# Performance work log

Measured on AMD Instinct MI355X. Metric: run time of the kernel, lower is better.

The kernel has to match this reference:

```python
import jax, jax.numpy as jnp
import numpy as np

C = 128        # attention channels (inner_channel)
OUT_C = 256    # bottleneck output channels (in_channel)
NEG = -10000000.0


def conv_bn_relu(x, W, scale, shift):
    """1x1 conv (no bias) + eval-mode BatchNorm folded to scale/shift + ReLU.
    x: [B, Cin, H, W], W: [Cout, Cin]."""
    y = jnp.einsum('oc,bchw->bohw', W, x)
    y = y * scale[None, :, None, None] + shift[None, :, None, None]
    return jax.nn.relu(y)


def setup_inputs() -> dict:
    key = jax.random.key(0)
    ks = jax.random.split(key, 20)
    B, H, W_, K = 4, 128, 128, 1024
    inp = {
        'query_feats': jax.random.normal(ks[0], (B, C, H, W_), jnp.float32),
        'key_feats':   jax.random.normal(ks[1], (B, C, K, 1), jnp.float32),
        'value_feats': jax.random.normal(ks[2], (B, C, K, 1), jnp.float32),
        'key_mask':    jax.random.randint(ks[3], (B, 1, K, 1), 0, 2).astype(bool),
    }
    s = 1.0 / np.sqrt(C)

    def mk(i, cin, cout):
        return (jax.random.normal(ks[i], (cout, cin), jnp.float32) * s,
                jnp.ones((cout,), jnp.float32),
                jnp.zeros((cout,), jnp.float32))

    inp['Wq1'], inp['sq1'], inp['bq1'] = mk(4, C, C)
    inp['Wq2'], inp['sq2'], inp['bq2'] = mk(5, C, C)
    inp['Wk1'], inp['sk1'], inp['bk1'] = mk(6, C, C)
    inp['Wk2'], inp['sk2'], inp['bk2'] = mk(7, C, C)
    inp['Wv'],  inp['sv'],  inp['bv']  = mk(8, C, C)
    inp['Wo'],  inp['so'],  inp['bo']  = mk(9, C, C)
    inp['Wb'],  inp['sb'],  inp['bb']  = mk(10, 2 * C, OUT_C)
    return inp


def reference(query_feats, key_feats, value_feats, key_mask,
              Wq1, sq1, bq1, Wq2, sq2, bq2,
              Wk1, sk1, bk1, Wk2, sk2, bk2,
              Wv, sv, bv, Wo, so, bo, Wb, sb, bb):
    B, _, H, W_ = query_feats.shape
    # projections (2 conv-bn-relu for q/k, 1 for v)
    q = conv_bn_relu(conv_bn_relu(query_feats, Wq1, sq1, bq1), Wq2, sq2, bq2)
    k = conv_bn_relu(conv_bn_relu(key_feats, Wk1, sk1, bk1), Wk2, sk2, bk2)
    v = conv_bn_relu(value_feats, Wv, sv, bv)

    q = q.reshape(B, C, -1).transpose(0, 2, 1)   # [B, HW, C]
    k = k.reshape(B, C, -1)                      # [B, C, K]
    v = v.reshape(B, C, -1).transpose(0, 2, 1)   # [B, K, C]

    sim = jnp.einsum('bqc,bck->bqk', q, k) * (C ** -0.5)   # [B, HW, K]
    m = key_mask.reshape(B, 1, -1).astype(sim.dtype)        # [B, 1, K]
    sim = sim * m + NEG * (1.0 - m)
    attn = jax.nn.softmax(sim, axis=-1)

    ctx = jnp.einsum('bqk,bkc->bqc', attn, v)               # [B, HW, C]
    ctx = ctx.transpose(0, 2, 1).reshape(B, C, H, W_)
    ctx = conv_bn_relu(ctx, Wo, so, bo)                     # out_project

    out = conv_bn_relu(jnp.concatenate([ctx, query_feats], axis=1), Wb, sb, bb)
    return out
```

## Files before the change

### kernel.cpp

```cpp
#include <hip/hip_runtime.h>
#include <hip/hip_bf16.h>

#define B_    4
#define C_    128
#define HW_   16384
#define K_    1024
#define SC2_  0.12751734f
#define NEGL_ (-1.4427e7f)
#define DTHR_ 8.0f

using bf16 = __hip_bfloat16;
typedef __bf16 b8v __attribute__((ext_vector_type(8)));
typedef __bf16 b4v __attribute__((ext_vector_type(4)));
typedef __bf16 b2v __attribute__((ext_vector_type(2)));
typedef float  f4v __attribute__((ext_vector_type(4)));

__device__ __forceinline__ b8v ldb8(const void* p) { return *(const b8v*)p; }

#define XSTRIDE 272
#define KSTRIDE 272
#define VSTRIDE 144

__device__ __forceinline__ b8v ldw8(const float* wp, float sc) {
    const float4 a = *(const float4*)wp;
    const float4 c = *(const float4*)(wp + 4);
    b8v r;
    r[0] = (__bf16)(a.x * sc); r[1] = (__bf16)(a.y * sc);
    r[2] = (__bf16)(a.z * sc); r[3] = (__bf16)(a.w * sc);
    r[4] = (__bf16)(c.x * sc); r[5] = (__bf16)(c.y * sc);
    r[6] = (__bf16)(c.z * sc); r[7] = (__bf16)(c.w * sc);
    return r;
}

__global__ __launch_bounds__(256, 2) void prep_kernel(
    const float* __restrict__ query, const float* __restrict__ key, const float* __restrict__ val,
    const float* __restrict__ Wq1, const float* __restrict__ sq1,
    const float* __restrict__ Wq2, const float* __restrict__ sq2,
    const float* __restrict__ Wo,  const float* __restrict__ so,
    const float* __restrict__ Wb,  const float* __restrict__ sb,
    const float* __restrict__ Wk1, const float* __restrict__ sk1, const float* __restrict__ bk1,
    const float* __restrict__ Wk2, const float* __restrict__ sk2, const float* __restrict__ bk2,
    const float* __restrict__ Wv,  const float* __restrict__ sv_, const float* __restrict__ bv,
    bf16* __restrict__ qt, bf16* __restrict__ kbuf, bf16* __restrict__ vbuf,
    __bf16* __restrict__ Wq1p, __bf16* __restrict__ Wq2p,
    __bf16* __restrict__ Wop,  __bf16* __restrict__ Wbp)
{
    __shared__ __align__(16) char SM[69632];
    const int blk = blockIdx.x, t = threadIdx.x;

    if (blk < 32) {
        const int b = blk >> 3, n0 = (blk & 7) * 128;
        const int w = t >> 6, lane = t & 63;
        const int pl = lane & 15, quad = lane >> 4;
        const int ob = 32 * w;
        const int plT = t & 63, cg = t >> 6;
        char*    Xs  = SM;
        __bf16*  Ys  = (__bf16*)(SM + 34816);
        float*   Tmp = (float*)(SM + 34816);

        auto transpose_in = [&](const float* src) {
#pragma unroll
            for (int h = 0; h < 2; ++h) {
                const int p0 = n0 + h * 64;
#pragma unroll 4
                for (int i2 = 0; i2 < 32; ++i2) {
                    const int c = cg * 32 + i2;
                    Tmp[plT * 129 + c] = src[(size_t)(b * 128 + c) * K_ + p0 + plT];
                }
                __syncthreads();
#pragma unroll 4
                for (int it = 0; it < 16; ++it) {
                    const int p = it * 4 + cg;
                    b2v pk2;
                    pk2[0] = (__bf16)Tmp[p * 129 + 2 * plT];
                    pk2[1] = (__bf16)Tmp[p * 129 + 2 * plT + 1];
                    *(b2v*)(Xs + (h * 64 + p) * XSTRIDE + 4 * plT) = pk2;
                }
                __syncthreads();
            }
        };

        transpose_in(key);
        b8v W1f[2][4], W2f[2][4];
#pragma unroll
        for (int mt = 0; mt < 2; ++mt)
#pragma unroll
            for (int s = 0; s < 4; ++s) {
                const int row = ob + mt * 16 + pl;
                W1f[mt][s] = ldw8(Wk1 + row * 128 + s * 32 + quad * 8, sk1[row]);
                W2f[mt][s] = ldw8(Wk2 + row * 128 + s * 32 + quad * 8, sk2[row]);
            }
        {
            f4v acc[2][8];
#pragma unroll
            for (int mt = 0; mt < 2; ++mt)
#pragma unroll
                for (int nt = 0; nt < 8; ++nt) acc[mt][nt] = (f4v){0.f, 0.f, 0.f, 0.f};
#pragma unroll
            for (int s = 0; s < 4; ++s) {
                b8v Bf[8];
#pragma unroll
                for (int nt = 0; nt < 8; ++nt)
                    Bf[nt] = ldb8(Xs + (nt * 16 + pl) * XSTRIDE + s * 64 + quad * 16);
#pragma unroll
                for (int mt = 0; mt < 2; ++mt)
#pragma unroll
                    for (int nt = 0; nt < 8; ++nt)
                        acc[mt][nt] = __builtin_amdgcn_mfma_f32_16x16x32_bf16(W1f[mt][s], Bf[nt], acc[mt][nt], 0, 0, 0);
            }
#pragma unroll
            for (int mt = 0; mt < 2; ++mt) {
                const float4 s4 = *(const float4*)(bk1 + ob + mt * 16 + quad * 4);
                const float shf[4] = {s4.x, s4.y, s4.z, s4.w};
#pragma unroll
                for (int nt = 0; nt < 8; ++nt) {
                    b4v y;
#pragma unroll
                    for (int r = 0; r < 4; ++r) y[r] = (__bf16)fmaxf(acc[mt][nt][r] + shf[r], 0.f);
                    *(b4v*)&Ys[(nt * 16 + pl) * 136 + ob + mt * 16 + quad * 4] = y;
                }
            }
        }
        __syncthreads();
        {
            f4v acc2[2][8];
#pragma unroll
            for (int mt = 0; mt < 2; ++mt)
#pragma unroll
                for (int nt = 0; nt < 8; ++nt) acc2[mt][nt] = (f4v){0.f, 0.f, 0.f, 0.f};
#pragma unroll
            for (int s = 0; s < 4; ++s) {
                b8v Bf[8];
#pragma unroll
                for (int nt = 0; nt < 8; ++nt)
                    Bf[nt] = *(const b8v*)&Ys[(nt * 16 + pl) * 136 + s * 32 + quad * 8];
#pragma unroll
                for (int mt = 0; mt < 2; ++mt)
#pragma unroll
                    for (int nt = 0; nt < 8; ++nt)
                        acc2[mt][nt] = __builtin_amdgcn_mfma_f32_16x16x32_bf16(W2f[mt][s], Bf[nt], acc2[mt][nt], 0, 0, 0);
            }
            bf16* kdst = kbuf + ((size_t)b * K_ + n0) * 128;
#pragma unroll
            for (int mt = 0; mt < 2; ++mt) {
                const float4 s4 = *(const float4*)(bk2 + ob + mt * 16 + quad * 4);
                const float shf[4] = {s4.x, s4.y, s4.z, s4.w};
#pragma unroll
                for (int nt = 0; nt < 8; ++nt) {
                    b4v y;
#pragma unroll
                    for (int r = 0; r < 4; ++r) y[r] = (__bf16)fmaxf(acc2[mt][nt][r] + shf[r], 0.f);
                    *(b4v*)(kdst + (size_t)(nt * 16 + pl) * 128 + ob + mt * 16 + quad * 4) = y;
                }
            }
        }
        __syncthreads();

        transpose_in(val);
        b8v Wvf[2][4];
#pragma unroll
        for (int mt = 0; mt < 2; ++mt)
#pragma unroll
            for (int s = 0; s < 4; ++s) {
                const int row = ob + mt * 16 + pl;
                Wvf[mt][s] = ldw8(Wv + row * 128 + s * 32 + quad * 8, sv_[row]);
            }
        {
            f4v acc[2][8];
#pragma unroll
            for (int mt = 0; mt < 2; ++mt)
#pragma unroll
                for (int nt = 0; nt < 8; ++nt) acc[mt][nt] = (f4v){0.f, 0.f, 0.f, 0.f};
#pragma unroll
            for (int s = 0; s < 4; ++s) {
                b8v Bf[8];
#pragma unroll
                for (int nt = 0; nt < 8; ++nt)
                    Bf[nt] = ldb8(Xs + (nt * 16 + pl) * XSTRIDE + s * 64 + quad * 16);
#pragma unroll
                for (int mt = 0; mt < 2; ++mt)
#pragma unroll
                    for (int nt = 0; nt < 8; ++nt)
                        acc[mt][nt] = __builtin_amdgcn_mfma_f32_16x16x32_bf16(Wvf[mt][s], Bf[nt], acc[mt][nt], 0, 0, 0);
            }
            bf16* vdst = vbuf + (size_t)b * 128 * K_;
#pragma unroll
            for (int mt = 0; mt < 2; ++mt) {
                const float4 s4 = *(const float4*)(bv + ob + mt * 16 + quad * 4);
                const float shf[4] = {s4.x, s4.y, s4.z, s4.w};
#pragma unroll
                for (int nt = 0; nt < 8; ++nt)
#pragma unroll
                    for (int r = 0; r < 4; ++r)
                        vdst[(size_t)(ob + mt * 16 + quad * 4 + r) * K_ + n0 + nt * 16 + pl]
                            = __float2bfloat16(fmaxf(acc[mt][nt][r] + shf[r], 0.f));
            }
        }
    } else if (blk < 1056) {
        float* Xs2 = (float*)SM;
        const int i = blk - 32;
        const int b = i >> 8, p0 = (i & 255) * 64;
        const int pl = t & 63, cg = t >> 6;
#pragma unroll 4
        for (int i2 = 0; i2 < 32; ++i2) {
            const int c = cg * 32 + i2;
            Xs2[pl * 129 + c] = query[(size_t)(b * 128 + c) * HW_ + p0 + pl];
        }
        __syncthreads();
#pragma unroll 4
        for (int it = 0; it < 16; ++it) {
            const int p = it * 4 + cg;
            b2v pk2;
            pk2[0] = (__bf16)Xs2[p * 129 + 2 * pl];
            pk2[1] = (__bf16)Xs2[p * 129 + 2 * pl + 1];
            *(b2v*)(qt + ((size_t)b * HW_ + p0 + p) * 128 + 2 * pl) = pk2;
        }
    } else {
        const int idx = (blk - 1056) * 256 + t;
        if (idx < 16384)      { Wq1p[idx] = (__bf16)(Wq1[idx] * sq1[idx >> 7]); }
        else if (idx < 32768) { const int i2 = idx - 16384; Wq2p[i2] = (__bf16)(Wq2[i2] * sq2[i2 >> 7]); }
        else if (idx < 49152) { const int i2 = idx - 32768; Wop[i2]  = (__bf16)(Wo[i2]  * so[i2 >> 7]); }
        else                  { const int i2 = idx - 49152; Wbp[i2]  = (__bf16)(Wb[i2]  * sb[i2 >> 8]); }
    }
}

__global__ __launch_bounds__(256, 2) void mega_kernel(
    const bf16* __restrict__ qt, const bf16* __restrict__ kbuf, const bf16* __restrict__ vbuf,
    const int* __restrict__ mask,
    const __bf16* __restrict__ Wq1p, const float* __restrict__ bq1,
    const __bf16* __restrict__ Wq2p, const float* __restrict__ bq2,
    const __bf16* __restrict__ Wop,  const float* __restrict__ bo,
    const __bf16* __restrict__ Wbp,  const float* __restrict__ bb,
    float* __restrict__ out)
{
    __shared__ __align__(16) char S[75776];

    const int t = threadIdx.x, w = t >> 6, lane = t & 63;
    const int pl = lane & 15, quad = lane >> 4;
    const int n0 = blockIdx.x * 128;
    const int b  = blockIdx.y;
    const int ob = 32 * w;

    char*   RA  = S;
    __bf16* RAh = (__bf16*)S;
    __bf16* RBh = (__bf16*)(S + 34816);
    char* xl = RA + (t >> 4) * XSTRIDE + (t & 15) * 16;

    {
        const char* qg = (const char*)(qt + ((size_t)b * HW_ + n0) * 128) + t * 16;
#pragma unroll
        for (int i = 0; i < 8; ++i)
            *(float4*)(xl + i * 16 * XSTRIDE) = *(const float4*)(qg + i * 4096);
    }
    {
        b8v W1f[2][4], W2f[2][4];
#pragma unroll
        for (int mt = 0; mt < 2; ++mt)
#pragma unroll
            for (int s = 0; s < 4; ++s) {
                W1f[mt][s] = ldb8(Wq1p + (ob + mt * 16 + pl) * 128 + s * 32 + quad * 8);
                W2f[mt][s] = ldb8(Wq2p + (ob + mt * 16 + pl) * 128 + s * 32 + quad * 8);
            }
        __syncthreads();

        f4v a1[2][8];
#pragma unroll
        for (int mt = 0; mt < 2; ++mt)
#pragma unroll
            for (int nt = 0; nt < 8; ++nt) a1[mt][nt] = (f4v){0.f, 0.f, 0.f, 0.f};
#pragma unroll
        for (int s = 0; s < 4; ++s) {
            b8v Bf[8];
#pragma unroll
            for (int nt = 0; nt < 8; ++nt)
                Bf[nt] = ldb8(RA + (nt * 16 + pl) * XSTRIDE + s * 64 + quad * 16);
#pragma unroll
            for (int mt = 0; mt < 2; ++mt)
#pragma unroll
                for (int nt = 0; nt < 8; ++nt)
                    a1[mt][nt] = __builtin_amdgcn_mfma_f32_16x16x32_bf16(W1f[mt][s], Bf[nt], a1[mt][nt], 0, 0, 0);
        }
#pragma unroll
        for (int mt = 0; mt < 2; ++mt) {
            const float4 s4 = *(const float4*)(bq1 + ob + mt * 16 + quad * 4);
            const float shf[4] = {s4.x, s4.y, s4.z, s4.w};
#pragma unroll
            for (int nt = 0; nt < 8; ++nt) {
                b4v y;
#pragma unroll
                for (int r = 0; r < 4; ++r) y[r] = (__bf16)fmaxf(a1[mt][nt][r] + shf[r], 0.f);
                *(b4v*)&RBh[(nt * 16 + pl) * 136 + ob + mt * 16 + quad * 4] = y;
            }
        }
        __syncthreads();

        f4v a2[2][8];
#pragma unroll
        for (int mt = 0; mt < 2; ++mt)
#pragma unroll
            for (int nt = 0; nt < 8; ++nt) a2[mt][nt] = (f4v){0.f, 0.f, 0.f, 0.f};
#pragma unroll
        for (int s = 0; s < 4; ++s) {
            b8v Bf[8];
#pragma unroll
            for (int nt = 0; nt < 8; ++nt)
                Bf[nt] = *(const b8v*)&RBh[(nt * 16 + pl) * 136 + s * 32 + quad * 8];
#pragma unroll
            for (int mt = 0; mt < 2; ++mt)
#pragma unroll
                for (int nt = 0; nt < 8; ++nt)
                    a2[mt][nt] = __builtin_amdgcn_mfma_f32_16x16x32_bf16(W2f[mt][s], Bf[nt], a2[mt][nt], 0, 0, 0);
        }
#pragma unroll
        for (int mt = 0; mt < 2; ++mt) {
            const float4 s4 = *(const float4*)(bq2 + ob + mt * 16 + quad * 4);
            const float shf[4] = {s4.x, s4.y, s4.z, s4.w};
#pragma unroll
            for (int nt = 0; nt < 8; ++nt) {
                b4v y;
#pragma unroll
                for (int r = 0; r < 4; ++r) y[r] = (__bf16)fmaxf(a2[mt][nt][r] + shf[r], 0.f);
                *(b4v*)&RAh[(nt * 16 + pl) * 136 + ob + mt * 16 + quad * 4] = y;
            }
        }
        __syncthreads();
    }

    b8v qf0[4], qf1[4];
#pragma unroll
    for (int s = 0; s < 4; ++s) {
        qf0[s] = ldb8(RA + (w * 32 + pl) * XSTRIDE + s * 64 + quad * 16);
        qf1[s] = ldb8(RA + (w * 32 + 16 + pl) * XSTRIDE + s * 64 + quad * 16);
    }
    __syncthreads();

    float* bias = (float*)S;
    char* kt0 = S + 4096;
    char* kt1 = S + 21504;
    char* vt0 = S + 38912;
    char* vt1 = S + 57344;

    const bf16* kpt = kbuf + (size_t)b * K_ * 128;
    const bf16* vpt = vbuf + (size_t)b * 128 * K_;
    const char* kg = (const char*)kpt + t * 16;
    const char* vg = (const char*)(vpt + (size_t)(t >> 3) * K_) + (t & 7) * 16;
    const int klo = (t >> 4) * KSTRIDE + (t & 15) * 16;
    const int vj  = t & 7;
    const int vlo = (t >> 3) * VSTRIDE + (vj >> 2) * 64 + (vj & 1) * 32 + ((vj >> 1) & 1) * 8;

    float4 kr[4], vr[4];

#define ISSUE_LOADS(chunk)                                            \
    { const char* kgn = kg + (chunk) * 16384;                         \
      const char* vgn = vg + (chunk) * 128;                           \
      kr[0] = *(const float4*)(kgn);                                  \
      kr[1] = *(const float4*)(kgn + 4096);                           \
      kr[2] = *(const float4*)(kgn + 8192);                           \
      kr[3] = *(const float4*)(kgn + 12288);                          \
      vr[0] = *(const float4*)(vgn);                                  \
      vr[1] = *(const float4*)(vgn + 65536);                          \
      vr[2] = *(const float4*)(vgn + 131072);                         \
      vr[3] = *(const float4*)(vgn + 196608); }

#define STAGE_WRITES(ktd, vtd)                                        \
    { char* klp = (ktd) + klo;                                        \
      *(float4*)(klp)                = kr[0];                         \
      *(float4*)(klp + 16 * KSTRIDE) = kr[1];                         \
      *(float4*)(klp + 32 * KSTRIDE) = kr[2];                         \
      *(float4*)(klp + 48 * KSTRIDE) = kr[3];                         \
      char* vlp = (vtd) + vlo;                                        \
      *(float2*)(vlp)                     = make_float2(vr[0].x, vr[0].y); \
      *(float2*)(vlp + 16)                = make_float2(vr[0].z, vr[0].w); \
      *(float2*)(vlp + 32 * VSTRIDE)      = make_float2(vr[1].x, vr[1].y); \
      *(float2*)(vlp + 32 * VSTRIDE + 16) = make_float2(vr[1].z, vr[1].w); \
      *(float2*)(vlp + 64 * VSTRIDE)      = make_float2(vr[2].x, vr[2].y); \
      *(float2*)(vlp + 64 * VSTRIDE + 16) = make_float2(vr[2].z, vr[2].w); \
      *(float2*)(vlp + 96 * VSTRIDE)      = make_float2(vr[3].x, vr[3].y); \
      *(float2*)(vlp + 96 * VSTRIDE + 16) = make_float2(vr[3].z, vr[3].w); }

#define RAW_BARRIER()                                                 \
    __builtin_amdgcn_sched_barrier(0);                                \
    asm volatile("s_waitcnt lgkmcnt(0)" ::: "memory");                \
    __builtin_amdgcn_s_barrier();                                     \
    __builtin_amdgcn_sched_barrier(0);

    ISSUE_LOADS(0)
    for (int i2 = t; i2 < K_; i2 += 256)
        bias[i2] = (mask[b * K_ + i2] != 0) ? 0.f : NEGL_;
    STAGE_WRITES(kt0, vt0)
    ISSUE_LOADS(1)

    f4v ac0[8], ac1[8];
#pragma unroll
    for (int i = 0; i < 8; ++i) { ac0[i] = (f4v){0.f,0.f,0.f,0.f}; ac1[i] = (f4v){0.f,0.f,0.f,0.f}; }
    float mrun0 = -3.0e38f, mrun1 = -3.0e38f, lrun0 = 0.f, lrun1 = 0.f;

    RAW_BARRIER()

#pragma unroll 2
    for (int ch = 0; ch < 16; ++ch) {
        const char* ktc = (ch & 1) ? kt1 : kt0;
        const char* vtc = (ch & 1) ? vt1 : vt0;
        const int k0 = ch * 64;

        f4v sv0[4], sv1[4];
        __builtin_amdgcn_s_setprio(1);
#pragma unroll
        for (int kt = 0; kt < 4; ++kt) {
            f4v a0 = (f4v){0.f,0.f,0.f,0.f}, a1 = (f4v){0.f,0.f,0.f,0.f};
            const char* krow = ktc + (kt * 16 + pl) * KSTRIDE + quad * 16;
#pragma unroll
            for (int s = 0; s < 4; ++s) {
                const b8v kf = ldb8(krow + s * 64);
                a0 = __builtin_amdgcn_mfma_f32_16x16x32_bf16(kf, qf0[s], a0, 0, 0, 0);
                a1 = __builtin_amdgcn_mfma_f32_16x16x32_bf16(kf, qf1[s], a1, 0, 0, 0);
            }
            const float4 b4 = *(const float4*)&bias[k0 + kt * 16 + quad * 4];
            const float bb4[4] = {b4.x, b4.y, b4.z, b4.w};
#pragma unroll
            for (int r = 0; r < 4; ++r) { sv0[kt][r] = a0[r] * SC2_ + bb4[r];
                                          sv1[kt][r] = a1[r] * SC2_ + bb4[r]; }
        }
        __builtin_amdgcn_s_setprio(0);

        if (ch < 15) {
            if (ch & 1) { STAGE_WRITES(kt0, vt0) } else { STAGE_WRITES(kt1, vt1) }
            if (ch < 14) ISSUE_LOADS(ch + 2)
        }

        float ml0 = sv0[0][0], ml1 = sv1[0][0];
#pragma unroll
        for (int kt = 0; kt < 4; ++kt)
#pragma unroll
            for (int r = 0; r < 4; ++r) { ml0 = fmaxf(ml0, sv0[kt][r]); ml1 = fmaxf(ml1, sv1[kt][r]); }
        ml0 = fmaxf(ml0, __shfl_xor(ml0, 16, 64)); ml0 = fmaxf(ml0, __shfl_xor(ml0, 32, 64));
        ml1 = fmaxf(ml1, __shfl_xor(ml1, 16, 64)); ml1 = fmaxf(ml1, __shfl_xor(ml1, 32, 64));

        if (__any((ml0 > mrun0 + DTHR_) || (ml1 > mrun1 + DTHR_))) {
            const float mn0 = fmaxf(mrun0, ml0), mn1 = fmaxf(mrun1, ml1);
            const float al0 = exp2f(mrun0 - mn0), al1 = exp2f(mrun1 - mn1);
            lrun0 *= al0; lrun1 *= al1;
            mrun0 = mn0;  mrun1 = mn1;
            float ar0[4], ar1[4];
#pragma unroll
            for (int r = 0; r < 4; ++r) { ar0[r] = __shfl(al0, quad * 4 + r, 64);
                                          ar1[r] = __shfl(al1, quad * 4 + r, 64); }
#pragma unroll
            for (int ct = 0; ct < 8; ++ct)
#pragma unroll
                for (int r = 0; r < 4; ++r) { ac0[ct][r] *= ar0[r]; ac1[ct][r] *= ar1[r]; }
        }

        b4v pk0[4], pk1[4];
        float rs0 = 0.f, rs1 = 0.f;
#pragma unroll
        for (int kt = 0; kt < 4; ++kt)
#pragma unroll
            for (int r = 0; r < 4; ++r) {
                const float p0 = exp2f(sv0[kt][r] - mrun0); rs0 += p0; pk0[kt][r] = (__bf16)p0;
                const float p1 = exp2f(sv1[kt][r] - mrun1); rs1 += p1; pk1[kt][r] = (__bf16)p1;
            }
        rs0 += __shfl_xor(rs0, 16, 64); rs0 += __shfl_xor(rs0, 32, 64);
        rs1 += __shfl_xor(rs1, 16, 64); rs1 += __shfl_xor(rs1, 32, 64);
        lrun0 += rs0; lrun1 += rs1;

        const b8v A00 = __builtin_shufflevector(pk0[0], pk0[1], 0, 1, 2, 3, 4, 5, 6, 7);
        const b8v A01 = __builtin_shufflevector(pk0[2], pk0[3], 0, 1, 2, 3, 4, 5, 6, 7);
        const b8v A10 = __builtin_shufflevector(pk1[0], pk1[1], 0, 1, 2, 3, 4, 5, 6, 7);
        const b8v A11 = __builtin_shufflevector(pk1[2], pk1[3], 0, 1, 2, 3, 4, 5, 6, 7);
        __builtin_amdgcn_s_setprio(1);
#pragma unroll
        for (int ct = 0; ct < 8; ++ct) {
            const char* vrow = vtc + (ct * 16 + pl) * VSTRIDE + quad * 16;
            const b8v B0 = ldb8(vrow);
            const b8v B1 = ldb8(vrow + 64);
            ac0[ct] = __builtin_amdgcn_mfma_f32_16x16x32_bf16(A00, B0, ac0[ct], 0, 0, 0);
            ac0[ct] = __builtin_amdgcn_mfma_f32_16x16x32_bf16(A01, B1, ac0[ct], 0, 0, 0);
            ac1[ct] = __builtin_amdgcn_mfma_f32_16x16x32_bf16(A10, B0, ac1[ct], 0, 0, 0);
            ac1[ct] = __builtin_amdgcn_mfma_f32_16x16x32_bf16(A11, B1, ac1[ct], 0, 0, 0);
        }
        __builtin_amdgcn_s_setprio(0);

        RAW_BARRIER()
    }
#undef ISSUE_LOADS
#undef STAGE_WRITES
#undef RAW_BARRIER

    {
        float inv0[4], inv1[4];
#pragma unroll
        for (int r = 0; r < 4; ++r) { inv0[r] = 1.f / __shfl(lrun0, quad * 4 + r, 64);
                                      inv1[r] = 1.f / __shfl(lrun1, quad * 4 + r, 64); }
#pragma unroll
        for (int ct = 0; ct < 8; ++ct)
#pragma unroll
            for (int r = 0; r < 4; ++r) {
                RAh[(w * 32 + quad * 4 + r) * 136 + ct * 16 + pl]      = (__bf16)(ac0[ct][r] * inv0[r]);
                RAh[(w * 32 + 16 + quad * 4 + r) * 136 + ct * 16 + pl] = (__bf16)(ac1[ct][r] * inv1[r]);
            }
    }
    __syncthreads();

    b8v Wof[2][4];
#pragma unroll
    for (int mt = 0; mt < 2; ++mt)
#pragma unroll
        for (int s = 0; s < 4; ++s)
            Wof[mt][s] = ldb8(Wop + (ob + mt * 16 + pl) * 128 + s * 32 + quad * 8);

    const char* qg2 = (const char*)(qt + ((size_t)b * HW_ + n0) * 128) + t * 16;
    float4 q_s0 = *(const float4*)(qg2);
    float4 q_s1 = *(const float4*)(qg2 + 4096);
    float4 q_s2 = *(const float4*)(qg2 + 8192);
    float4 q_s3 = *(const float4*)(qg2 + 12288);
    float4 q_s4 = *(const float4*)(qg2 + 16384);
    float4 q_s5 = *(const float4*)(qg2 + 20480);
    float4 q_s6 = *(const float4*)(qg2 + 24576);
    float4 q_s7 = *(const float4*)(qg2 + 28672);

    {
        f4v f1[2][8];
#pragma unroll
        for (int mt = 0; mt < 2; ++mt)
#pragma unroll
            for (int nt = 0; nt < 8; ++nt) f1[mt][nt] = (f4v){0.f, 0.f, 0.f, 0.f};
#pragma unroll
        for (int s = 0; s < 4; ++s) {
            b8v Bf[8];
#pragma unroll
            for (int nt = 0; nt < 8; ++nt)
                Bf[nt] = ldb8(RA + (nt * 16 + pl) * XSTRIDE + s * 64 + quad * 16);
#pragma unroll
            for (int mt = 0; mt < 2; ++mt)
#pragma unroll
                for (int nt = 0; nt < 8; ++nt)
                    f1[mt][nt] = __builtin_amdgcn_mfma_f32_16x16x32_bf16(Wof[mt][s], Bf[nt], f1[mt][nt], 0, 0, 0);
        }
#pragma unroll
        for (int mt = 0; mt < 2; ++mt) {
            const float4 s4 = *(const float4*)(bo + ob + mt * 16 + quad * 4);
            const float shf[4] = {s4.x, s4.y, s4.z, s4.w};
#pragma unroll
            for (int nt = 0; nt < 8; ++nt) {
                b4v y;
#pragma unroll
                for (int r = 0; r < 4; ++r) y[r] = (__bf16)fmaxf(f1[mt][nt][r] + shf[r], 0.f);
                *(b4v*)&RBh[(nt * 16 + pl) * 136 + ob + mt * 16 + quad * 4] = y;
            }
        }
    }
    __syncthreads();

    *(float4*)(xl)                 = q_s0;
    *(float4*)(xl + 16 * XSTRIDE)  = q_s1;
    *(float4*)(xl + 32 * XSTRIDE)  = q_s2;
    *(float4*)(xl + 48 * XSTRIDE)  = q_s3;
    *(float4*)(xl + 64 * XSTRIDE)  = q_s4;
    *(float4*)(xl + 80 * XSTRIDE)  = q_s5;
    *(float4*)(xl + 96 * XSTRIDE)  = q_s6;
    *(float4*)(xl + 112 * XSTRIDE) = q_s7;
    __syncthreads();

    {
        f4v f2[4][8];
#pragma unroll
        for (int mt = 0; mt < 4; ++mt)
#pragma unroll
            for (int nt = 0; nt < 8; ++nt) f2[mt][nt] = (f4v){0.f, 0.f, 0.f, 0.f};
#pragma unroll
        for (int ks = 0; ks < 8; ++ks) {
            b8v Af[4];
#pragma unroll
            for (int mt = 0; mt < 4; ++mt)
                Af[mt] = ldb8(Wbp + (size_t)(64 * w + mt * 16 + pl) * 256 + ks * 32 + quad * 8);
            b8v Bf[8];
            if (ks < 4) {
#pragma unroll
                for (int nt = 0; nt < 8; ++nt)
                    Bf[nt] = *(const b8v*)&RBh[(nt * 16 + pl) * 136 + ks * 32 + quad * 8];
            } else {
#pragma unroll
                for (int nt = 0; nt < 8; ++nt)
                    Bf[nt] = ldb8(RA + (nt * 16 + pl) * XSTRIDE + (ks - 4) * 64 + quad * 16);
            }
#pragma unroll
            for (int mt = 0; mt < 4; ++mt)
#pragma unroll
                for (int nt = 0; nt < 8; ++nt)
                    f2[mt][nt] = __builtin_amdgcn_mfma_f32_16x16x32_bf16(Af[mt], Bf[nt], f2[mt][nt], 0, 0, 0);
        }
#pragma unroll
        for (int mt = 0; mt < 4; ++mt) {
            const float4 s4 = *(const float4*)(bb + 64 * w + mt * 16 + quad * 4);
            const float shf[4] = {s4.x, s4.y, s4.z, s4.w};
#pragma unroll
            for (int nt = 0; nt < 8; ++nt)
#pragma unroll
                for (int r = 0; r < 4; ++r)
                    out[(size_t)(b * 256 + 64 * w + mt * 16 + quad * 4 + r) * HW_ + n0 + nt * 16 + pl]
                        = fmaxf(f2[mt][nt][r] + shf[r], 0.f);
        }
    }
}

extern "C" void kernel_launch(void* const* d_in, const int* in_sizes, int n_in,
                              void* d_out, int out_size, void* d_ws, size_t ws_size,
                              hipStream_t stream)
{
    const float* query = (const float*)d_in[0];
    const float* key   = (const float*)d_in[1];
    const float* val   = (const float*)d_in[2];
    const int*   mask  = (const int*)  d_in[3];
    const float* Wq1 = (const float*)d_in[4];  const float* sq1 = (const float*)d_in[5];  const float* bq1 = (const float*)d_in[6];
    const float* Wq2 = (const float*)d_in[7];  const float* sq2 = (const float*)d_in[8];  const float* bq2 = (const float*)d_in[9];
    const float* Wk1 = (const float*)d_in[10]; const float* sk1 = (const float*)d_in[11]; const float* bk1 = (const float*)d_in[12];
    const float* Wk2 = (const float*)d_in[13]; const float* sk2 = (const float*)d_in[14]; const float* bk2 = (const float*)d_in[15];
    const float* Wv  = (const float*)d_in[16]; const float* sv  = (const float*)d_in[17]; const float* bv  = (const float*)d_in[18];
    const float* Wo  = (const float*)d_in[19]; const float* so  = (const float*)d_in[20]; const float* bo  = (const float*)d_in[21];
    const float* Wb  = (const float*)d_in[22]; const float* sb  = (const float*)d_in[23]; const float* bb  = (const float*)d_in[24];

    char* ws = (char*)d_ws;
    bf16*   qt   = (bf16*)(ws);
    bf16*   kbuf = (bf16*)(ws + (16u << 20));
    bf16*   vbuf = (bf16*)(ws + (17u << 20));
    char*   wbase = ws + (18u << 20);
    __bf16* Wq1p = (__bf16*)(wbase);
    __bf16* Wq2p = (__bf16*)(wbase + (32u << 10));
    __bf16* Wop  = (__bf16*)(wbase + (64u << 10));
    __bf16* Wbp  = (__bf16*)(wbase + (96u << 10));
    float* outp = (float*)d_out;

    prep_kernel<<<1504, 256, 0, stream>>>(
        query, key, val,
        Wq1, sq1, Wq2, sq2, Wo, so, Wb, sb,
        Wk1, sk1, bk1, Wk2, sk2, bk2, Wv, sv, bv,
        qt, kbuf, vbuf, Wq1p, Wq2p, Wop, Wbp);
    mega_kernel<<<dim3(HW_ / 128, B_), 256, 0, stream>>>(
        qt, kbuf, vbuf, mask,
        Wq1p, bq1, Wq2p, bq2, Wop, bo, Wbp, bb, outp);
}
```

Before: 231.7 us.

## Replace double-buffered K/V LDS staging with single buffer and register prefetch

Drops the two-slot LDS ping-pong for K and V tiles and uses one LDS tile per operand. Each chunk's data, held in registers, is written to LDS and followed by a barrier before the next chunk's global loads are issued. The V tile switches from a permuted 8-byte-store layout to plain 16-byte stores with a smaller stride, and reads it back as two 4-element loads per operand. This cuts LDS use and store instruction count, but adds a barrier per chunk and shortens the overlap of global loads with compute.

```diff
diff --git a/kernel.cpp b/kernel.cpp
--- a/kernel.cpp
+++ b/kernel.cpp
@@ -16,10 +16,11 @@
 typedef float  f4v __attribute__((ext_vector_type(4)));
 
 __device__ __forceinline__ b8v ldb8(const void* p) { return *(const b8v*)p; }
+__device__ __forceinline__ b4v ldb4(const void* p) { return *(const b4v*)p; }
 
 #define XSTRIDE 272
 #define KSTRIDE 272
-#define VSTRIDE 144
+#define VSTRIDE 136
 
 __device__ __forceinline__ b8v ldw8(const float* wp, float sc) {
     const float4 a = *(const float4*)wp;
@@ -233,7 +234,7 @@
     const __bf16* __restrict__ Wbp,  const float* __restrict__ bb,
     float* __restrict__ out)
 {
-    __shared__ __align__(16) char S[75776];
+    __shared__ __align__(16) char S[69632];
 
     const int t = threadIdx.x, w = t >> 6, lane = t & 63;
     const int pl = lane & 15, quad = lane >> 4;
@@ -335,48 +336,32 @@
     __syncthreads();
 
     float* bias = (float*)S;
-    char* kt0 = S + 4096;
-    char* kt1 = S + 21504;
-    char* vt0 = S + 38912;
-    char* vt1 = S + 57344;
+    char* ktile = S + 4096;
+    char* vtile = S + 34816;
+
+    for (int i2 = t; i2 < K_; i2 += 256)
+        bias[i2] = (mask[b * K_ + i2] != 0) ? 0.f : NEGL_;
 
     const bf16* kpt = kbuf + (size_t)b * K_ * 128;
     const bf16* vpt = vbuf + (size_t)b * 128 * K_;
     const char* kg = (const char*)kpt + t * 16;
     const char* vg = (const char*)(vpt + (size_t)(t >> 3) * K_) + (t & 7) * 16;
-    const int klo = (t >> 4) * KSTRIDE + (t & 15) * 16;
-    const int vj  = t & 7;
-    const int vlo = (t >> 3) * VSTRIDE + (vj >> 2) * 64 + (vj & 1) * 32 + ((vj >> 1) & 1) * 8;
-
-    float4 kr[4], vr[4];
-
-#define ISSUE_LOADS(chunk)                                            \
-    { const char* kgn = kg + (chunk) * 16384;                         \
-      const char* vgn = vg + (chunk) * 128;                           \
-      kr[0] = *(const float4*)(kgn);                                  \
-      kr[1] = *(const float4*)(kgn + 4096);                           \
-      kr[2] = *(const float4*)(kgn + 8192);                           \
-      kr[3] = *(const float4*)(kgn + 12288);                          \
-      vr[0] = *(const float4*)(vgn);                                  \
-      vr[1] = *(const float4*)(vgn + 65536);                          \
-      vr[2] = *(const float4*)(vgn + 131072);                         \
-      vr[3] = *(const float4*)(vgn + 196608); }
-
-#define STAGE_WRITES(ktd, vtd)                                        \
-    { char* klp = (ktd) + klo;                                        \
-      *(float4*)(klp)                = kr[0];                         \
-      *(float4*)(klp + 16 * KSTRIDE) = kr[1];                         \
-      *(float4*)(klp + 32 * KSTRIDE) = kr[2];                         \
-      *(float4*)(klp + 48 * KSTRIDE) = kr[3];                         \
-      char* vlp = (vtd) + vlo;                                        \
-      *(float2*)(vlp)                     = make_float2(vr[0].x, vr[0].y); \
-      *(float2*)(vlp + 16)                = make_float2(vr[0].z, vr[0].w); \
-      *(float2*)(vlp + 32 * VSTRIDE)      = make_float2(vr[1].x, vr[1].y); \
-      *(float2*)(vlp + 32 * VSTRIDE + 16) = make_float2(vr[1].z, vr[1].w); \
-      *(float2*)(vlp + 64 * VSTRIDE)      = make_float2(vr[2].x, vr[2].y); \
-      *(float2*)(vlp + 64 * VSTRIDE + 16) = make_float2(vr[2].z, vr[2].w); \
-      *(float2*)(vlp + 96 * VSTRIDE)      = make_float2(vr[3].x, vr[3].y); \
-      *(float2*)(vlp + 96 * VSTRIDE + 16) = make_float2(vr[3].z, vr[3].w); }
+    char* kl = ktile + (t >> 4) * KSTRIDE + (t & 15) * 16;
+    char* vl = vtile + (t >> 3) * VSTRIDE + (t & 7) * 16;
+
+    float4 k_r0 = *(const float4*)(kg);
+    float4 k_r1 = *(const float4*)(kg + 4096);
+    float4 k_r2 = *(const float4*)(kg + 8192);
+    float4 k_r3 = *(const float4*)(kg + 12288);
+    float4 v_r0 = *(const float4*)(vg);
+    float4 v_r1 = *(const float4*)(vg + 65536);
+    float4 v_r2 = *(const float4*)(vg + 131072);
+    float4 v_r3 = *(const float4*)(vg + 196608);
+
+    f4v ac0[8], ac1[8];
+#pragma unroll
+    for (int i = 0; i < 8; ++i) { ac0[i] = (f4v){0.f,0.f,0.f,0.f}; ac1[i] = (f4v){0.f,0.f,0.f,0.f}; }
+    float mrun0 = -3.0e38f, mrun1 = -3.0e38f, lrun0 = 0.f, lrun1 = 0.f;
 
 #define RAW_BARRIER()                                                 \
     __builtin_amdgcn_sched_barrier(0);                                \
@@ -384,31 +369,38 @@
     __builtin_amdgcn_s_barrier();                                     \
     __builtin_amdgcn_sched_barrier(0);
 
-    ISSUE_LOADS(0)
-    for (int i2 = t; i2 < K_; i2 += 256)
-        bias[i2] = (mask[b * K_ + i2] != 0) ? 0.f : NEGL_;
-    STAGE_WRITES(kt0, vt0)
-    ISSUE_LOADS(1)
-
-    f4v ac0[8], ac1[8];
-#pragma unroll
-    for (int i = 0; i < 8; ++i) { ac0[i] = (f4v){0.f,0.f,0.f,0.f}; ac1[i] = (f4v){0.f,0.f,0.f,0.f}; }
-    float mrun0 = -3.0e38f, mrun1 = -3.0e38f, lrun0 = 0.f, lrun1 = 0.f;
-
-    RAW_BARRIER()
-
-#pragma unroll 2
-    for (int ch = 0; ch < 16; ++ch) {
-        const char* ktc = (ch & 1) ? kt1 : kt0;
-        const char* vtc = (ch & 1) ? vt1 : vt0;
-        const int k0 = ch * 64;
+    for (int chunk = 0; chunk < 16; ++chunk) {
+        const int k0 = chunk * 64;
+
+        *(float4*)(kl)                = k_r0;
+        *(float4*)(kl + 16 * KSTRIDE) = k_r1;
+        *(float4*)(kl + 32 * KSTRIDE) = k_r2;
+        *(float4*)(kl + 48 * KSTRIDE) = k_r3;
+        *(float4*)(vl)                = v_r0;
+        *(float4*)(vl + 32 * VSTRIDE) = v_r1;
+        *(float4*)(vl + 64 * VSTRIDE) = v_r2;
+        *(float4*)(vl + 96 * VSTRIDE) = v_r3;
+        RAW_BARRIER()
+
+        if (chunk < 15) {
+            const char* kgn = kg + (chunk + 1) * 16384;
+            const char* vgn = vg + (chunk + 1) * 128;
+            k_r0 = *(const float4*)(kgn);
+            k_r1 = *(const float4*)(kgn + 4096);
+            k_r2 = *(const float4*)(kgn + 8192);
+            k_r3 = *(const float4*)(kgn + 12288);
+            v_r0 = *(const float4*)(vgn);
+            v_r1 = *(const float4*)(vgn + 65536);
+            v_r2 = *(const float4*)(vgn + 131072);
+            v_r3 = *(const float4*)(vgn + 196608);
+        }
 
         f4v sv0[4], sv1[4];
         __builtin_amdgcn_s_setprio(1);
 #pragma unroll
         for (int kt = 0; kt < 4; ++kt) {
             f4v a0 = (f4v){0.f,0.f,0.f,0.f}, a1 = (f4v){0.f,0.f,0.f,0.f};
-            const char* krow = ktc + (kt * 16 + pl) * KSTRIDE + quad * 16;
+            const char* krow = ktile + (kt * 16 + pl) * KSTRIDE + quad * 16;
 #pragma unroll
             for (int s = 0; s < 4; ++s) {
                 const b8v kf = ldb8(krow + s * 64);
@@ -422,11 +414,6 @@
                                           sv1[kt][r] = a1[r] * SC2_ + bb4[r]; }
         }
         __builtin_amdgcn_s_setprio(0);
-
-        if (ch < 15) {
-            if (ch & 1) { STAGE_WRITES(kt0, vt0) } else { STAGE_WRITES(kt1, vt1) }
-            if (ch < 14) ISSUE_LOADS(ch + 2)
-        }
 
         float ml0 = sv0[0][0], ml1 = sv1[0][0];
 #pragma unroll
@@ -471,9 +458,9 @@
         __builtin_amdgcn_s_setprio(1);
 #pragma unroll
         for (int ct = 0; ct < 8; ++ct) {
-            const char* vrow = vtc + (ct * 16 + pl) * VSTRIDE + quad * 16;
-            const b8v B0 = ldb8(vrow);
-            const b8v B1 = ldb8(vrow + 64);
+            const char* vrow = vtile + (ct * 16 + pl) * VSTRIDE + quad * 8;
+            const b8v B0 = __builtin_shufflevector(ldb4(vrow),      ldb4(vrow + 32), 0, 1, 2, 3, 4, 5, 6, 7);
+            const b8v B1 = __builtin_shufflevector(ldb4(vrow + 64), ldb4(vrow + 96), 0, 1, 2, 3, 4, 5, 6, 7);
             ac0[ct] = __builtin_amdgcn_mfma_f32_16x16x32_bf16(A00, B0, ac0[ct], 0, 0, 0);
             ac0[ct] = __builtin_amdgcn_mfma_f32_16x16x32_bf16(A01, B1, ac0[ct], 0, 0, 0);
             ac1[ct] = __builtin_amdgcn_mfma_f32_16x16x32_bf16(A10, B0, ac1[ct], 0, 0, 0);
@@ -483,8 +470,6 @@
 
         RAW_BARRIER()
     }
-#undef ISSUE_LOADS
-#undef STAGE_WRITES
 #undef RAW_BARRIER
 
     {
```

After: 231.3 us. About the same (-0.2%).
